# Performance work log

Measured on AMD Instinct MI355X. Metric: run time of the kernel, lower is better.

## Reference

```python
import jax, jax.numpy as jnp
import numpy as np

EPS_LN = 1e-6
EPS_L2 = 1e-12

def _ln(x, g, b):
    m = jnp.mean(x, axis=-1, keepdims=True)
    v = jnp.mean((x - m) ** 2, axis=-1, keepdims=True)
    return (x - m) / jnp.sqrt(v + EPS_LN) * g + b

def _l2norm(x, axis):
    n = jnp.sqrt(jnp.sum(x * x, axis=axis, keepdims=True))
    return x / jnp.maximum(n, EPS_L2)

def setup_inputs() -> dict:
    key = jax.random.key(0)
    ks = jax.random.split(key, 5)
    b, h, w, d = 32, 64, 64, 192
    td, ad = 768, 128
    return dict(
        x=jax.random.normal(ks[0], (b, h, w, d), jnp.float32),
        token=jax.random.normal(ks[1], (b, td), jnp.float32),
        p=jax.random.uniform(ks[2], (b, 1), jnp.float32),
        alpha=jnp.zeros((1,), jnp.float32),
        ln1_g=jnp.ones((td,), jnp.float32), ln1_b=jnp.zeros((td,), jnp.float32),
        w_tok=jax.random.normal(ks[3], (td, ad), jnp.float32) * 0.02,
        b_tok=jnp.zeros((ad,), jnp.float32),
        ln2_g=jnp.ones((d,), jnp.float32), ln2_b=jnp.zeros((d,), jnp.float32),
        w_x=jax.random.normal(ks[4], (d, ad), jnp.float32) * 0.02,
        b_x=jnp.zeros((ad,), jnp.float32),
        ln3_g=jnp.ones((d,), jnp.float32), ln3_b=jnp.zeros((d,), jnp.float32),
    )

def reference(x, token, p, alpha, ln1_g, ln1_b, w_tok, b_tok, ln2_g, ln2_b, w_x, b_x, ln3_g, ln3_b):
    b, h, w, d = x.shape
    # token_proj(norm1(token)) : [b, attn_dims]
    tok = jax.nn.gelu(_ln(token, ln1_g, ln1_b) @ w_tok + b_tok, approximate=False)
    # x_proj(norm2(x flattened)) : [b, hw, attn_dims]
    xf = x.reshape(b, h * w, d)
    x_ = jax.nn.gelu(_ln(xf, ln2_g, ln2_b) @ w_x + b_x, approximate=False)
    # L2-normalized skinny dot-product attention -> [b, hw]
    xn = _l2norm(x_, axis=2)
    tn = _l2norm(tok, axis=1)
    attn = p * jnp.einsum('bnk,bk->bn', xn, tn) * jnp.exp(alpha)  # p:[b,1] broadcasts
    attn = attn.reshape(b, h, w)
    # residual: 0.5*x + norm3(x * attn)
    out = 0.5 * x + _ln(x * attn[..., None], ln3_g, ln3_b)
    return out
```

## Files before the change

### kernel.cpp

```cpp
#include <hip/hip_runtime.h>
#include <math.h>

typedef _Float16 f16;
typedef f16  v8h __attribute__((ext_vector_type(8)));
typedef float v4f __attribute__((ext_vector_type(4)));

#define EPS_LN 1e-6f
#define GELU_K 0.70710678118654752440f
#define LO_SCALE 65536.0f
#define LO_INV   (1.0f/65536.0f)

#define WS_TN 98304

#define LSTR 216
#define KOFF (64*216)

__device__ __forceinline__ void split16(float v, f16& hi, f16& lo){
  hi = (f16)v;
  lo = (f16)((v - (float)hi) * LO_SCALE);
}

__global__ __launch_bounds__(64) void prep_w(const float* __restrict__ wx, uint4* __restrict__ wf){
  const int S = blockIdx.x >> 3, t = blockIdx.x & 7, l = threadIdx.x;
  const int n  = (t << 4) + (l & 15);
  const int k0 = (S << 5) + ((l >> 4) << 3);
  union { v8h v; uint4 u; } H, L;
  #pragma unroll
  for(int j = 0; j < 8; ++j){
    float v = wx[(size_t)(k0 + j)*128 + n];
    f16 h, lo; split16(v, h, lo);
    H.v[j] = h; L.v[j] = lo;
  }
  wf[(0*6 + S)*512 + t*64 + l] = H.u;
  wf[(1*6 + S)*512 + t*64 + l] = L.u;
}

__global__ __launch_bounds__(256) void tok_kernel(
    const float* __restrict__ token, const float* __restrict__ p, const float* __restrict__ alpha,
    const float* __restrict__ g1, const float* __restrict__ b1,
    const float* __restrict__ w_tok, const float* __restrict__ b_tok,
    float* __restrict__ tn_out)
{
  __shared__ float ln[768];
  __shared__ float part[256];
  __shared__ float yv[128];
  __shared__ float rs1[4], rs2[4];
  const int b = blockIdx.x;
  const int t = threadIdx.x;
  const int lane = t & 63, wid = t >> 6;
  const float* tok = token + b*768;

  float v0 = tok[t], v1 = tok[t+256], v2 = tok[t+512];
  float s1 = v0+v1+v2, s2 = v0*v0+v1*v1+v2*v2;
  #pragma unroll
  for(int m = 1; m < 64; m <<= 1){ s1 += __shfl_xor(s1,m,64); s2 += __shfl_xor(s2,m,64); }
  if(lane == 0){ rs1[wid] = s1; rs2[wid] = s2; }
  __syncthreads();
  float S1 = rs1[0]+rs1[1]+rs1[2]+rs1[3];
  float S2 = rs2[0]+rs2[1]+rs2[2]+rs2[3];
  float mean = S1*(1.f/768.f);
  float var  = S2*(1.f/768.f) - mean*mean;
  float rstd = rsqrtf(var + EPS_LN);
  ln[t]       = (v0-mean)*rstd*g1[t]       + b1[t];
  ln[t + 256] = (v1-mean)*rstd*g1[t + 256] + b1[t + 256];
  ln[t + 512] = (v2-mean)*rstd*g1[t + 512] + b1[t + 512];
  __syncthreads();

  const int k  = t & 127;
  const int d0 = (t >> 7) * 384;
  const float* wp = w_tok + (size_t)d0*128 + k;
  float a0 = 0.f, a1 = 0.f, a2 = 0.f, a3 = 0.f;
  #pragma unroll 4
  for(int d = 0; d < 384; d += 4){
    a0 = fmaf(ln[d0+d+0], wp[(size_t)(d+0)*128], a0);
    a1 = fmaf(ln[d0+d+1], wp[(size_t)(d+1)*128], a1);
    a2 = fmaf(ln[d0+d+2], wp[(size_t)(d+2)*128], a2);
    a3 = fmaf(ln[d0+d+3], wp[(size_t)(d+3)*128], a3);
  }
  part[t] = (a0+a1)+(a2+a3);
  __syncthreads();
  if(t < 128){
    float y = part[t] + part[t + 128] + b_tok[k];
    y = 0.5f*y*(1.f + erff(y*GELU_K));
    yv[t] = y;
  }
  __syncthreads();
  float ss = (t < 128) ? yv[t]*yv[t] : 0.f;
  #pragma unroll
  for(int m = 1; m < 64; m <<= 1) ss += __shfl_xor(ss, m, 64);
  if(lane == 0) rs1[wid] = ss;
  __syncthreads();
  float SS = rs1[0]+rs1[1]+rs1[2]+rs1[3];
  float scale = p[b]*expf(alpha[0]) / fmaxf(sqrtf(SS), 1e-12f);
  if(t < 128) tn_out[b*128 + t] = yv[t]*scale;
}

__global__ __launch_bounds__(256, 2) void x_kernel(
    const float* __restrict__ x, const float* __restrict__ g2, const float* __restrict__ b2,
    const uint4* __restrict__ wf, const float* __restrict__ bx,
    const float* __restrict__ g3, const float* __restrict__ b3,
    const float* __restrict__ tn, float* __restrict__ out)
{
  __shared__ f16   llds[2*64*LSTR];
  __shared__ float pss[4][64], pdt[4][64];

  const int t = threadIdx.x, lane = t & 63, wv = t >> 6;
  const int q = lane & 3, r = lane >> 2;
  const size_t row0 = (size_t)blockIdx.x * 64;
  const int bidx = (int)(row0 >> 12);
  const int myrow = wv*16 + r;
  const float* xrow = x + (row0 + myrow)*192 + q*48;

  v8h Bh[6][2], Bl[6][2];
  #pragma unroll
  for(int S = 0; S < 6; ++S){
    #pragma unroll
    for(int u = 0; u < 2; ++u){
      Bh[S][u] = *(const v8h*)&wf[(0*6 + S)*512 + (2*wv + u)*64 + lane];
      Bl[S][u] = *(const v8h*)&wf[(1*6 + S)*512 + (2*wv + u)*64 + lane];
    }
  }

  float xv[48];
  #pragma unroll
  for(int i = 0; i < 12; ++i) *(float4*)&xv[i*4] = *(const float4*)(xrow + i*4);
  float s1 = 0.f, s2 = 0.f;
  #pragma unroll
  for(int i = 0; i < 48; ++i){ s1 += xv[i]; s2 = fmaf(xv[i], xv[i], s2); }
  s1 += __shfl_xor(s1, 1, 64); s1 += __shfl_xor(s1, 2, 64);
  s2 += __shfl_xor(s2, 1, 64); s2 += __shfl_xor(s2, 2, 64);
  const float mu   = s1 * (1.f/192.f);
  const float var  = s2 * (1.f/192.f) - mu*mu;
  const float rstd = rsqrtf(var + EPS_LN);

  {
    const float* g2p = g2 + q*48;
    const float* b2p = b2 + q*48;
    const int base = myrow*LSTR + q*48;
    #pragma unroll
    for(int i = 0; i < 48; i += 8){
      union { v8h v; uint4 u; } H, L;
      #pragma unroll
      for(int j = 0; j < 8; ++j){
        float lv = (xv[i+j] - mu)*rstd*g2p[i+j] + b2p[i+j];
        f16 h, lo; split16(lv, h, lo);
        H.v[j] = h; L.v[j] = lo;
      }
      *(uint4*)&llds[       base + i] = H.u;
      *(uint4*)&llds[KOFF + base + i] = L.u;
    }
  }
  __syncthreads();

  const int n0 = lane & 15, quad = lane >> 4;
  const float* tnb = tn + bidx*128;
  #pragma unroll
  for(int mt = 0; mt < 4; ++mt){
    v4f c1[2], c2[2];
    #pragma unroll
    for(int u = 0; u < 2; ++u){ c1[u] = (v4f){0,0,0,0}; c2[u] = (v4f){0,0,0,0}; }
    #pragma unroll
    for(int S = 0; S < 6; ++S){
      const int ab = (mt*16 + n0)*LSTR + quad*8 + S*32;
      v8h ah = *(v8h*)&llds[ab];
      v8h al = *(v8h*)&llds[KOFF + ab];
      #pragma unroll
      for(int u = 0; u < 2; ++u){
        c1[u] = __builtin_amdgcn_mfma_f32_16x16x32_f16(ah, Bh[S][u], c1[u], 0, 0, 0);
        c2[u] = __builtin_amdgcn_mfma_f32_16x16x32_f16(al, Bh[S][u], c2[u], 0, 0, 0);
        c2[u] = __builtin_amdgcn_mfma_f32_16x16x32_f16(ah, Bl[S][u], c2[u], 0, 0, 0);
      }
    }
    float ssv[4] = {0,0,0,0}, dtv[4] = {0,0,0,0};
    #pragma unroll
    for(int u = 0; u < 2; ++u){
      const int col = n0 + 16*(2*wv + u);
      const float bxv = bx[col], tnv = tnb[col];
      #pragma unroll
      for(int g = 0; g < 4; ++g){
        float y = fmaf(c2[u][g], LO_INV, c1[u][g]) + bxv;
        y = 0.5f*y*(1.f + erff(y*GELU_K));
        ssv[g] = fmaf(y, y,   ssv[g]);
        dtv[g] = fmaf(y, tnv, dtv[g]);
      }
    }
    #pragma unroll
    for(int g = 0; g < 4; ++g){
      #pragma unroll
      for(int m = 1; m < 16; m <<= 1){
        ssv[g] += __shfl_xor(ssv[g], m, 64);
        dtv[g] += __shfl_xor(dtv[g], m, 64);
      }
    }
    if(n0 == 0){
      #pragma unroll
      for(int g = 0; g < 4; ++g){
        pss[wv][mt*16 + quad*4 + g] = ssv[g];
        pdt[wv][mt*16 + quad*4 + g] = dtv[g];
      }
    }
  }
  __syncthreads();

  const float SSt = pss[0][myrow] + pss[1][myrow] + pss[2][myrow] + pss[3][myrow];
  const float DTt = pdt[0][myrow] + pdt[1][myrow] + pdt[2][myrow] + pdt[3][myrow];
  const float attn = DTt / fmaxf(sqrtf(SSt), 1e-12f);
  const float rd = rsqrtf(attn*attn*var + EPS_LN);
  const float am = attn * rd;
  const float* g3p = g3 + q*48;
  const float* b3p = b3 + q*48;
  float* orow = out + (row0 + myrow)*192 + q*48;
  #pragma unroll
  for(int i = 0; i < 12; ++i){
    float4 gv = *(const float4*)(g3p + i*4);
    float4 bv = *(const float4*)(b3p + i*4);
    float4 o;
    o.x = fmaf(0.5f, xv[i*4+0], fmaf(am*(xv[i*4+0]-mu), gv.x, bv.x));
    o.y = fmaf(0.5f, xv[i*4+1], fmaf(am*(xv[i*4+1]-mu), gv.y, bv.y));
    o.z = fmaf(0.5f, xv[i*4+2], fmaf(am*(xv[i*4+2]-mu), gv.z, bv.z));
    o.w = fmaf(0.5f, xv[i*4+3], fmaf(am*(xv[i*4+3]-mu), gv.w, bv.w));
    *(float4*)(orow + i*4) = o;
  }
}

extern "C" void kernel_launch(void* const* d_in, const int* in_sizes, int n_in,
                              void* d_out, int out_size, void* d_ws, size_t ws_size,
                              hipStream_t stream) {
  const float* x     = (const float*)d_in[0];
  const float* token = (const float*)d_in[1];
  const float* p     = (const float*)d_in[2];
  const float* alpha = (const float*)d_in[3];
  const float* g1    = (const float*)d_in[4];
  const float* b1    = (const float*)d_in[5];
  const float* wtok  = (const float*)d_in[6];
  const float* btok  = (const float*)d_in[7];
  const float* g2    = (const float*)d_in[8];
  const float* b2    = (const float*)d_in[9];
  const float* wx    = (const float*)d_in[10];
  const float* bx    = (const float*)d_in[11];
  const float* g3    = (const float*)d_in[12];
  const float* b3    = (const float*)d_in[13];

  uint4* wf = (uint4*)d_ws;
  float* tn = (float*)((char*)d_ws + WS_TN);
  float* outf = (float*)d_out;

  prep_w<<<48, 64, 0, stream>>>(wx, wf);
  tok_kernel<<<32, 256, 0, stream>>>(token, p, alpha, g1, b1, wtok, btok, tn);
  x_kernel<<<2048, 256, 0, stream>>>(x, g2, b2, wf, bx, g3, b3, tn, outf);
}
```

Baseline: 267.7 us.

## Stop holding x rows in registers; reload from global to cut VGPR pressure

The x_kernel no longer keeps each thread's 48 x values in registers across the whole kernel. It streams x once for the statistics, reloads it for the LN2 staging and again for the final output. The B-fragment register load moves after the LDS staging, and loops are partially unrolled (unroll 1 or 2) to cut register pressure. The aim is lower VGPR use and latency hiding, with possibly more waves per SIMD. The cost is reading x from global memory three times instead of once, which leans on the cache in a memory-bound kernel, and less unrolling in the MFMA loop.

```diff
diff --git a/kernel.cpp b/kernel.cpp
--- a/kernel.cpp
+++ b/kernel.cpp
@@ -111,24 +111,15 @@
   const int myrow = wv*16 + r;
   const float* xrow = x + (row0 + myrow)*192 + q*48;
 
-  v8h Bh[6][2], Bl[6][2];
-  #pragma unroll
-  for(int S = 0; S < 6; ++S){
-    #pragma unroll
-    for(int u = 0; u < 2; ++u){
-      Bh[S][u] = *(const v8h*)&wf[(0*6 + S)*512 + (2*wv + u)*64 + lane];
-      Bl[S][u] = *(const v8h*)&wf[(1*6 + S)*512 + (2*wv + u)*64 + lane];
-    }
-  }
-
-  float xv[48];
-  #pragma unroll
-  for(int i = 0; i < 12; ++i) *(float4*)&xv[i*4] = *(const float4*)(xrow + i*4);
   float s1 = 0.f, s2 = 0.f;
-  #pragma unroll
-  for(int i = 0; i < 48; ++i){ s1 += xv[i]; s2 = fmaf(xv[i], xv[i], s2); }
-  s1 += __shfl_xor(s1, 1, 64); s1 += __shfl_xor(s1, 2, 64);
-  s2 += __shfl_xor(s2, 1, 64); s2 += __shfl_xor(s2, 2, 64);
+  #pragma unroll 4
+  for(int i = 0; i < 12; ++i){
+    float4 v = *(const float4*)(xrow + i*4);
+    s1 += (v.x + v.y) + (v.z + v.w);
+    s2 = fmaf(v.x,v.x, fmaf(v.y,v.y, fmaf(v.z,v.z, fmaf(v.w,v.w, s2))));
+  }
+  s1 += __shfl_xor(s1,1,64); s1 += __shfl_xor(s1,2,64);
+  s2 += __shfl_xor(s2,1,64); s2 += __shfl_xor(s2,2,64);
   const float mu   = s1 * (1.f/192.f);
   const float var  = s2 * (1.f/192.f) - mu*mu;
   const float rstd = rsqrtf(var + EPS_LN);
@@ -137,52 +128,78 @@
     const float* g2p = g2 + q*48;
     const float* b2p = b2 + q*48;
     const int base = myrow*LSTR + q*48;
-    #pragma unroll
+    #pragma unroll 1
     for(int i = 0; i < 48; i += 8){
+      float4 xa = *(const float4*)(xrow + i);
+      float4 xb = *(const float4*)(xrow + i + 4);
+      float4 ga = *(const float4*)(g2p + i);
+      float4 gb = *(const float4*)(g2p + i + 4);
+      float4 ba = *(const float4*)(b2p + i);
+      float4 bb = *(const float4*)(b2p + i + 4);
+      float lv0 = (xa.x-mu)*rstd*ga.x + ba.x;
+      float lv1 = (xa.y-mu)*rstd*ga.y + ba.y;
+      float lv2 = (xa.z-mu)*rstd*ga.z + ba.z;
+      float lv3 = (xa.w-mu)*rstd*ga.w + ba.w;
+      float lv4 = (xb.x-mu)*rstd*gb.x + bb.x;
+      float lv5 = (xb.y-mu)*rstd*gb.y + bb.y;
+      float lv6 = (xb.z-mu)*rstd*gb.z + bb.z;
+      float lv7 = (xb.w-mu)*rstd*gb.w + bb.w;
       union { v8h v; uint4 u; } H, L;
-      #pragma unroll
-      for(int j = 0; j < 8; ++j){
-        float lv = (xv[i+j] - mu)*rstd*g2p[i+j] + b2p[i+j];
-        f16 h, lo; split16(lv, h, lo);
-        H.v[j] = h; L.v[j] = lo;
-      }
+      f16 h, lo;
+      split16(lv0,h,lo); H.v[0]=h; L.v[0]=lo;
+      split16(lv1,h,lo); H.v[1]=h; L.v[1]=lo;
+      split16(lv2,h,lo); H.v[2]=h; L.v[2]=lo;
+      split16(lv3,h,lo); H.v[3]=h; L.v[3]=lo;
+      split16(lv4,h,lo); H.v[4]=h; L.v[4]=lo;
+      split16(lv5,h,lo); H.v[5]=h; L.v[5]=lo;
+      split16(lv6,h,lo); H.v[6]=h; L.v[6]=lo;
+      split16(lv7,h,lo); H.v[7]=h; L.v[7]=lo;
       *(uint4*)&llds[       base + i] = H.u;
       *(uint4*)&llds[KOFF + base + i] = L.u;
     }
   }
+
+  v8h Bh[6][2], Bl[6][2];
+  #pragma unroll
+  for(int S = 0; S < 6; ++S){
+    #pragma unroll
+    for(int u = 0; u < 2; ++u){
+      Bh[S][u] = *(const v8h*)&wf[(0*6 + S)*512 + (2*wv + u)*64 + lane];
+      Bl[S][u] = *(const v8h*)&wf[(1*6 + S)*512 + (2*wv + u)*64 + lane];
+    }
+  }
   __syncthreads();
 
   const int n0 = lane & 15, quad = lane >> 4;
   const float* tnb = tn + bidx*128;
-  #pragma unroll
+  const int col0 = n0 + 16*(2*wv);
+  const float bx0 = bx[col0],  bx1 = bx[col0 + 16];
+  const float tn0 = tnb[col0], tn1 = tnb[col0 + 16];
+  #pragma unroll 1
   for(int mt = 0; mt < 4; ++mt){
-    v4f c1[2], c2[2];
-    #pragma unroll
-    for(int u = 0; u < 2; ++u){ c1[u] = (v4f){0,0,0,0}; c2[u] = (v4f){0,0,0,0}; }
+    v4f c1a = (v4f){0,0,0,0}, c1b = (v4f){0,0,0,0};
+    v4f c2a = (v4f){0,0,0,0}, c2b = (v4f){0,0,0,0};
+    const int ab0 = (mt*16 + n0)*LSTR + quad*8;
     #pragma unroll
     for(int S = 0; S < 6; ++S){
-      const int ab = (mt*16 + n0)*LSTR + quad*8 + S*32;
-      v8h ah = *(v8h*)&llds[ab];
-      v8h al = *(v8h*)&llds[KOFF + ab];
-      #pragma unroll
-      for(int u = 0; u < 2; ++u){
-        c1[u] = __builtin_amdgcn_mfma_f32_16x16x32_f16(ah, Bh[S][u], c1[u], 0, 0, 0);
-        c2[u] = __builtin_amdgcn_mfma_f32_16x16x32_f16(al, Bh[S][u], c2[u], 0, 0, 0);
-        c2[u] = __builtin_amdgcn_mfma_f32_16x16x32_f16(ah, Bl[S][u], c2[u], 0, 0, 0);
-      }
-    }
-    float ssv[4] = {0,0,0,0}, dtv[4] = {0,0,0,0};
-    #pragma unroll
-    for(int u = 0; u < 2; ++u){
-      const int col = n0 + 16*(2*wv + u);
-      const float bxv = bx[col], tnv = tnb[col];
-      #pragma unroll
-      for(int g = 0; g < 4; ++g){
-        float y = fmaf(c2[u][g], LO_INV, c1[u][g]) + bxv;
-        y = 0.5f*y*(1.f + erff(y*GELU_K));
-        ssv[g] = fmaf(y, y,   ssv[g]);
-        dtv[g] = fmaf(y, tnv, dtv[g]);
-      }
+      v8h ah = *(v8h*)&llds[ab0 + S*32];
+      v8h al = *(v8h*)&llds[KOFF + ab0 + S*32];
+      c1a = __builtin_amdgcn_mfma_f32_16x16x32_f16(ah, Bh[S][0], c1a, 0, 0, 0);
+      c2a = __builtin_amdgcn_mfma_f32_16x16x32_f16(al, Bh[S][0], c2a, 0, 0, 0);
+      c2a = __builtin_amdgcn_mfma_f32_16x16x32_f16(ah, Bl[S][0], c2a, 0, 0, 0);
+      c1b = __builtin_amdgcn_mfma_f32_16x16x32_f16(ah, Bh[S][1], c1b, 0, 0, 0);
+      c2b = __builtin_amdgcn_mfma_f32_16x16x32_f16(al, Bh[S][1], c2b, 0, 0, 0);
+      c2b = __builtin_amdgcn_mfma_f32_16x16x32_f16(ah, Bl[S][1], c2b, 0, 0, 0);
+    }
+    float ssv[4], dtv[4];
+    #pragma unroll
+    for(int g = 0; g < 4; ++g){
+      float y0 = fmaf(c2a[g], LO_INV, c1a[g]) + bx0;
+      y0 = 0.5f*y0*(1.f + erff(y0*GELU_K));
+      float y1 = fmaf(c2b[g], LO_INV, c1b[g]) + bx1;
+      y1 = 0.5f*y1*(1.f + erff(y1*GELU_K));
+      ssv[g] = fmaf(y0, y0,  y1*y1);
+      dtv[g] = fmaf(y0, tn0, y1*tn1);
     }
     #pragma unroll
     for(int g = 0; g < 4; ++g){
@@ -210,15 +227,16 @@
   const float* g3p = g3 + q*48;
   const float* b3p = b3 + q*48;
   float* orow = out + (row0 + myrow)*192 + q*48;
-  #pragma unroll
+  #pragma unroll 2
   for(int i = 0; i < 12; ++i){
+    float4 xv = *(const float4*)(xrow + i*4);
     float4 gv = *(const float4*)(g3p + i*4);
     float4 bv = *(const float4*)(b3p + i*4);
     float4 o;
-    o.x = fmaf(0.5f, xv[i*4+0], fmaf(am*(xv[i*4+0]-mu), gv.x, bv.x));
-    o.y = fmaf(0.5f, xv[i*4+1], fmaf(am*(xv[i*4+1]-mu), gv.y, bv.y));
-    o.z = fmaf(0.5f, xv[i*4+2], fmaf(am*(xv[i*4+2]-mu), gv.z, bv.z));
-    o.w = fmaf(0.5f, xv[i*4+3], fmaf(am*(xv[i*4+3]-mu), gv.w, bv.w));
+    o.x = fmaf(0.5f, xv.x, fmaf(am*(xv.x-mu), gv.x, bv.x));
+    o.y = fmaf(0.5f, xv.y, fmaf(am*(xv.y-mu), gv.y, bv.y));
+    o.z = fmaf(0.5f, xv.z, fmaf(am*(xv.z-mu), gv.z, bv.z));
+    o.w = fmaf(0.5f, xv.w, fmaf(am*(xv.w-mu), gv.w, bv.w));
     *(float4*)(orow + i*4) = o;
   }
 }
```

After: 367.8 us. +37.4%, slower.
